# Kernel optimization log

Measured on AMD Instinct MI355X. Metric: run time of the kernel, lower is better.

Reference implementation:

```python
import jax, jax.numpy as jnp
import numpy as np

B, N = 128, 1024

def setup_inputs() -> dict:
    key = jax.random.key(0)
    k1, k2, k3 = jax.random.split(key, 3)
    m = jax.random.normal(k1, (B, N), dtype=jnp.float32)
    k = jax.random.normal(k2, (B, N, N), dtype=jnp.float32)
    targets = jax.random.randint(k3, (B,), 0, N, dtype=jnp.int64)
    return {"m": m, "k": k, "targets": targets}

def reference(m, k, targets):
    # cross_entropy: logsumexp(m) - m[targets]
    ce = jax.nn.logsumexp(m, axis=-1) - jnp.take_along_axis(m, targets[:, None], axis=-1)[:, 0]
    p = jax.nn.softmax(m, axis=-1)  # [B, N]
    # (k * (diag_embed(p) - outer(p))).sum((-2,-1))
    #   = sum_n k[b,n,n] * p[b,n]  -  p^T K p   (avoids materializing hess)
    diag_k = jnp.einsum('bnn->bn', k)                 # [B, N]
    diag_term = jnp.sum(diag_k * p, axis=-1)          # [B]
    quad_term = jnp.einsum('bn,bnm,bm->b', p, k, p)   # [B]
    return ce + 0.5 * (diag_term - quad_term)
```

## Files before the change

kernel.cpp:

```cpp
#include <hip/hip_runtime.h>

#define BB   128
#define NN   1024
#define RPB  16
#define ROWS (NN / RPB)

__global__ __launch_bounds__(256) void softmax_ce_kernel(
    const float* __restrict__ m, const int* __restrict__ targets,
    float* __restrict__ p, float* __restrict__ ce)
{
    const int b   = blockIdx.x;
    const int tid = threadIdx.x;
    const float* mb = m + (size_t)b * NN;

    float4 v = reinterpret_cast<const float4*>(mb)[tid];

    __shared__ float sred[4];

    float mx = fmaxf(fmaxf(v.x, v.y), fmaxf(v.z, v.w));
    #pragma unroll
    for (int off = 32; off > 0; off >>= 1) mx = fmaxf(mx, __shfl_down(mx, off));
    if ((tid & 63) == 0) sred[tid >> 6] = mx;
    __syncthreads();
    mx = fmaxf(fmaxf(sred[0], sred[1]), fmaxf(sred[2], sred[3]));
    __syncthreads();

    float e0 = expf(v.x - mx), e1 = expf(v.y - mx);
    float e2 = expf(v.z - mx), e3 = expf(v.w - mx);
    float s = (e0 + e1) + (e2 + e3);
    #pragma unroll
    for (int off = 32; off > 0; off >>= 1) s += __shfl_down(s, off);
    if ((tid & 63) == 0) sred[tid >> 6] = s;
    __syncthreads();
    s = (sred[0] + sred[1]) + (sred[2] + sred[3]);

    const float inv = 1.0f / s;
    float4 pv = make_float4(e0 * inv, e1 * inv, e2 * inv, e3 * inv);
    reinterpret_cast<float4*>(p + (size_t)b * NN)[tid] = pv;

    if (tid == 0) {
        const float lse = mx + logf(s);
        ce[b] = lse - mb[targets[b]];
    }
}

__global__ __launch_bounds__(256) void quad_kernel(
    const float* __restrict__ k, const float* __restrict__ p,
    float* __restrict__ partial)
{
    const int blk = blockIdx.x;
    const int b   = blk / RPB;
    const int rb  = blk % RPB;
    const int tid = threadIdx.x;

    __shared__ float sp[NN];
    reinterpret_cast<float4*>(sp)[tid] =
        reinterpret_cast<const float4*>(p + (size_t)b * NN)[tid];
    __syncthreads();

    const int   m0  = 4 * tid;
    const float pm0 = sp[m0], pm1 = sp[m0 + 1], pm2 = sp[m0 + 2], pm3 = sp[m0 + 3];

    const int n0 = rb * ROWS;
    const float4* kp =
        reinterpret_cast<const float4*>(k + ((size_t)b * NN + n0) * NN) + tid;

    float acc = 0.0f;
    #pragma unroll 4
    for (int i = 0; i < ROWS; ++i) {
        const int n  = n0 + i;
        float4 k4    = kp[(size_t)i * (NN / 4)];
        float  pn    = sp[n];
        float  d0 = (n == m0    ) ? 1.0f : 0.0f;
        float  d1 = (n == m0 + 1) ? 1.0f : 0.0f;
        float  d2 = (n == m0 + 2) ? 1.0f : 0.0f;
        float  d3 = (n == m0 + 3) ? 1.0f : 0.0f;
        acc += pn * (k4.x * (d0 - pm0) + k4.y * (d1 - pm1) +
                     k4.z * (d2 - pm2) + k4.w * (d3 - pm3));
    }

    #pragma unroll
    for (int off = 32; off > 0; off >>= 1) acc += __shfl_down(acc, off);
    __shared__ float sred[4];
    if ((tid & 63) == 0) sred[tid >> 6] = acc;
    __syncthreads();
    if (tid == 0) partial[blk] = (sred[0] + sred[1]) + (sred[2] + sred[3]);
}

__global__ void finalize_kernel(const float* __restrict__ ce,
                                const float* __restrict__ partial,
                                float* __restrict__ out)
{
    const int b = threadIdx.x;
    if (b < BB) {
        float s = 0.0f;
        #pragma unroll
        for (int r = 0; r < RPB; ++r) s += partial[b * RPB + r];
        out[b] = ce[b] + 0.5f * s;
    }
}

extern "C" void kernel_launch(void* const* d_in, const int* in_sizes, int n_in,
                              void* d_out, int out_size, void* d_ws, size_t ws_size,
                              hipStream_t stream)
{
    const float* m       = (const float*)d_in[0];
    const float* k       = (const float*)d_in[1];
    const int*   targets = (const int*)d_in[2];
    float*       out     = (float*)d_out;

    float* p       = (float*)d_ws;
    float* ce      = p + (size_t)BB * NN;
    float* partial = ce + BB;

    softmax_ce_kernel<<<BB, 256, 0, stream>>>(m, targets, p, ce);
    quad_kernel<<<BB * RPB, 256, 0, stream>>>(k, p, partial);
    finalize_kernel<<<1, 128, 0, stream>>>(ce, partial, out);
}
```

Baseline: 101.4 us.

## Fuse softmax into quadratic-form kernel and use nontemporal loads for k

Each quad block now recomputes the row softmax itself from m instead of reading p written by a separate kernel. This removes one kernel launch and the round-trip of p through global memory. The k stream is read with nontemporal loads and the loop unroll is raised from 4 to 8. The cost is that the 1024-element softmax is computed redundantly by all 16 blocks of each batch row.

```diff
diff --git a/kernel.cpp b/kernel.cpp
--- a/kernel.cpp
+++ b/kernel.cpp
@@ -5,17 +5,23 @@
 #define RPB  16
 #define ROWS (NN / RPB)
 
-__global__ __launch_bounds__(256) void softmax_ce_kernel(
-    const float* __restrict__ m, const int* __restrict__ targets,
-    float* __restrict__ p, float* __restrict__ ce)
+typedef float f4 __attribute__((ext_vector_type(4)));
+
+__global__ __launch_bounds__(256) void fused_quad_kernel(
+    const float* __restrict__ m, const float* __restrict__ k,
+    const int* __restrict__ targets,
+    float* __restrict__ ce, float* __restrict__ partial)
 {
-    const int b   = blockIdx.x;
+    const int blk = blockIdx.x;
+    const int b   = blk >> 4;
+    const int rb  = blk & (RPB - 1);
     const int tid = threadIdx.x;
+
+    __shared__ float sp[NN];
+    __shared__ float sred[4];
+
     const float* mb = m + (size_t)b * NN;
-
     float4 v = reinterpret_cast<const float4*>(mb)[tid];
-
-    __shared__ float sred[4];
 
     float mx = fmaxf(fmaxf(v.x, v.y), fmaxf(v.z, v.w));
     #pragma unroll
@@ -35,53 +41,34 @@
     s = (sred[0] + sred[1]) + (sred[2] + sred[3]);
 
     const float inv = 1.0f / s;
-    float4 pv = make_float4(e0 * inv, e1 * inv, e2 * inv, e3 * inv);
-    reinterpret_cast<float4*>(p + (size_t)b * NN)[tid] = pv;
-
-    if (tid == 0) {
-        const float lse = mx + logf(s);
-        ce[b] = lse - mb[targets[b]];
-    }
-}
-
-__global__ __launch_bounds__(256) void quad_kernel(
-    const float* __restrict__ k, const float* __restrict__ p,
-    float* __restrict__ partial)
-{
-    const int blk = blockIdx.x;
-    const int b   = blk / RPB;
-    const int rb  = blk % RPB;
-    const int tid = threadIdx.x;
-
-    __shared__ float sp[NN];
-    reinterpret_cast<float4*>(sp)[tid] =
-        reinterpret_cast<const float4*>(p + (size_t)b * NN)[tid];
+    const float pm0 = e0 * inv, pm1 = e1 * inv, pm2 = e2 * inv, pm3 = e3 * inv;
+    reinterpret_cast<float4*>(sp)[tid] = make_float4(pm0, pm1, pm2, pm3);
     __syncthreads();
 
-    const int   m0  = 4 * tid;
-    const float pm0 = sp[m0], pm1 = sp[m0 + 1], pm2 = sp[m0 + 2], pm3 = sp[m0 + 3];
+    if (rb == 0 && tid == 0)
+        ce[b] = mx + logf(s) - mb[targets[b]];
 
+    const int m0 = 4 * tid;
     const int n0 = rb * ROWS;
-    const float4* kp =
-        reinterpret_cast<const float4*>(k + ((size_t)b * NN + n0) * NN) + tid;
+    const f4* kp = reinterpret_cast<const f4*>(k + ((size_t)b * NN + n0) * NN) + tid;
 
     float acc = 0.0f;
-    #pragma unroll 4
+    #pragma unroll 8
     for (int i = 0; i < ROWS; ++i) {
-        const int n  = n0 + i;
-        float4 k4    = kp[(size_t)i * (NN / 4)];
-        float  pn    = sp[n];
-        float  d0 = (n == m0    ) ? 1.0f : 0.0f;
-        float  d1 = (n == m0 + 1) ? 1.0f : 0.0f;
-        float  d2 = (n == m0 + 2) ? 1.0f : 0.0f;
-        float  d3 = (n == m0 + 3) ? 1.0f : 0.0f;
+        const int n = n0 + i;
+        f4    k4 = __builtin_nontemporal_load(kp + (size_t)i * (NN / 4));
+        float pn = sp[n];
+        float d0 = (n == m0    ) ? 1.0f : 0.0f;
+        float d1 = (n == m0 + 1) ? 1.0f : 0.0f;
+        float d2 = (n == m0 + 2) ? 1.0f : 0.0f;
+        float d3 = (n == m0 + 3) ? 1.0f : 0.0f;
         acc += pn * (k4.x * (d0 - pm0) + k4.y * (d1 - pm1) +
                      k4.z * (d2 - pm2) + k4.w * (d3 - pm3));
     }
 
     #pragma unroll
     for (int off = 32; off > 0; off >>= 1) acc += __shfl_down(acc, off);
-    __shared__ float sred[4];
+    __syncthreads();
     if ((tid & 63) == 0) sred[tid >> 6] = acc;
     __syncthreads();
     if (tid == 0) partial[blk] = (sred[0] + sred[1]) + (sred[2] + sred[3]);
@@ -109,11 +96,9 @@
     const int*   targets = (const int*)d_in[2];
     float*       out     = (float*)d_out;
 
-    float* p       = (float*)d_ws;
-    float* ce      = p + (size_t)BB * NN;
+    float* ce      = (float*)d_ws;
     float* partial = ce + BB;
 
-    softmax_ce_kernel<<<BB, 256, 0, stream>>>(m, targets, p, ce);
-    quad_kernel<<<BB * RPB, 256, 0, stream>>>(k, p, partial);
+    fused_quad_kernel<<<BB * RPB, 256, 0, stream>>>(m, k, targets, ce, partial);
     finalize_kernel<<<1, 128, 0, stream>>>(ce, partial, out);
 }
```

Result: faster. 85.22 us (-16.0%).
